# Optimization experiments

Hardware: AMD Instinct MI355X
Metric: run time of the kernel (lower is better)

Reference implementation:

```python
import jax, jax.numpy as jnp
import numpy as np

VOCAB, EMBED, HIDDEN = 32000, 512, 1024
BATCH, SEQ = 32, 48
PAD = 0


def setup_inputs() -> dict:
    key = jax.random.key(0)
    ks = jax.random.split(key, 10)
    s = 0.02
    emb = jax.random.normal(ks[0], (VOCAB, EMBED), jnp.float32) * s
    emb = emb.at[PAD].set(0.0)  # padding_idx row zeroed
    return {
        "inputs": jax.random.randint(ks[1], (BATCH, SEQ), 0, VOCAB),
        "hidden": jax.random.normal(ks[2], (BATCH, HIDDEN), jnp.float32),
        "cell": jax.random.normal(ks[3], (BATCH, HIDDEN), jnp.float32),
        "emb": emb,
        "W_ih": jax.random.normal(ks[4], (4 * HIDDEN, EMBED), jnp.float32) * s,
        "W_hh": jax.random.normal(ks[5], (4 * HIDDEN, HIDDEN), jnp.float32) * s,
        "b_ih": jnp.zeros((4 * HIDDEN,), jnp.float32),
        "b_hh": jnp.zeros((4 * HIDDEN,), jnp.float32),
        "fc_W": jax.random.normal(ks[6], (VOCAB, HIDDEN), jnp.float32) * s,
        "fc_b": jnp.zeros((VOCAB,), jnp.float32),
        "generate_len": 50,
    }


def reference(inputs, hidden, cell, emb, W_ih, W_hh, b_ih, b_hh, fc_W, fc_b, generate_len):
    # Training-path forward (dropout treated as identity for determinism).
    x = emb[inputs]                      # [B, S, E]
    xs = jnp.transpose(x, (1, 0, 2))     # [S, B, E] time-major

    def step(carry, x_t):
        h, c = carry
        gates = x_t @ W_ih.T + b_ih + h @ W_hh.T + b_hh  # [B, 4H]
        i, f, g, o = jnp.split(gates, 4, axis=-1)
        c_new = jax.nn.sigmoid(f) * c + jax.nn.sigmoid(i) * jnp.tanh(g)
        h_new = jax.nn.sigmoid(o) * jnp.tanh(c_new)
        logits = h_new @ fc_W.T + fc_b                   # [B, V]
        return (h_new, c_new), logits

    _, out = jax.lax.scan(step, (hidden, cell), xs)      # [S, B, V]
    return jnp.transpose(out, (1, 0, 2))                 # [B, S, V]
```

## Files before the change

### kernel.cpp

```cpp
#include <hip/hip_runtime.h>
#include <stdint.h>


typedef unsigned short u16;
typedef __attribute__((ext_vector_type(8))) short bf16x8;
typedef __attribute__((ext_vector_type(4))) float floatx4;
struct alignas(8) us4 { u16 x, y, z, w; };

#define BATCH 32
#define SEQ   48
#define EMBED 512
#define HID   1024
#define VOCAB 32000
#define MROWS (SEQ * BATCH)

__device__ __forceinline__ u16 f2bf(float f) {
  unsigned u = __float_as_uint(f);
  u += 0x7FFF + ((u >> 16) & 1);
  return (u16)(u >> 16);
}

__device__ __forceinline__ floatx4 mfma16(bf16x8 a, bf16x8 b, floatx4 c) {
  return __builtin_amdgcn_mfma_f32_16x16x32_bf16(a, b, c, 0, 0, 0);
}

typedef __attribute__((address_space(1))) unsigned int as1_uint;
typedef __attribute__((address_space(3))) unsigned int as3_uint;
__device__ __forceinline__ void gl_lds16(const void* g, void* l) {
  __builtin_amdgcn_global_load_lds((as1_uint*)g, (as3_uint*)l, 16, 0, 0);
}

__device__ __forceinline__ float sigmoidf_(float x) {
  return 1.0f / (1.0f + __expf(-x));
}

__device__ __forceinline__ void ld_c16(bf16x8& d, const u16* p) {
  asm volatile("global_load_dwordx4 %0, %1, off sc0 sc1" : "=&v"(d) : "v"(p));
}
__device__ __forceinline__ void ld_n16(bf16x8& d, const u16* p) {
  asm volatile("global_load_dwordx4 %0, %1, off" : "=&v"(d) : "v"(p));
}

#define BAR_U32S 576

__global__ void cast_all_kernel(const float* __restrict__ s0, u16* __restrict__ d0, int n0,
                                const float* __restrict__ s1, u16* __restrict__ d1, int n1,
                                const float* __restrict__ s2, u16* __restrict__ d2, int n2,
                                const float* __restrict__ s3, u16* __restrict__ d3, int n3) {
  int i = blockIdx.x * blockDim.x + threadIdx.x;
  const float* src; u16* dst; int off;
  if (i < n0)                     { src = s0; dst = d0; off = i; }
  else if (i < n0 + n1)           { src = s1; dst = d1; off = i - n0; }
  else if (i < n0 + n1 + n2)      { src = s2; dst = d2; off = i - n0 - n1; }
  else if (i < n0 + n1 + n2 + n3) { src = s3; dst = d3; off = i - n0 - n1 - n2; }
  else return;
  float4 v = *(const float4*)(src + (size_t)off * 4);
  us4 o;
  o.x = f2bf(v.x); o.y = f2bf(v.y); o.z = f2bf(v.z); o.w = f2bf(v.w);
  *(us4*)(dst + (size_t)off * 4) = o;
}

__global__ void gather_kernel(const int* __restrict__ idx, const float* __restrict__ emb,
                              u16* __restrict__ X, unsigned* __restrict__ bar) {
  int bid = blockIdx.x;
  if (bid == 0) {
    for (int j = threadIdx.x; j < BAR_U32S; j += 128) bar[j] = 0u;
  }
  int s = bid >> 5, b = bid & 31;
  int t = idx[b * SEQ + s];
  const float* src = emb + (size_t)t * EMBED;
  u16* dst = X + (size_t)bid * EMBED;
  int e = threadIdx.x * 4;
  float4 v = *(const float4*)(src + e);
  us4 o;
  o.x = f2bf(v.x); o.y = f2bf(v.y); o.z = f2bf(v.z); o.w = f2bf(v.w);
  *(us4*)(dst + e) = o;
}

__global__ __launch_bounds__(256) void gemm_bt_kernel(
    const u16* __restrict__ A, const u16* __restrict__ B,
    const float* __restrict__ bias0, const float* __restrict__ bias1,
    float* __restrict__ C, int M, int N, int K) {
  __shared__ u16 As[128 * 64];
  __shared__ u16 Bs[128 * 64];

  const int tid = threadIdx.x;
  const int wave = tid >> 6, lane = tid & 63;
  const int l3 = lane >> 3, l7 = lane & 7;
  const int q = lane >> 4, rf = lane & 15;
  const int tn = blockIdx.x, tm = blockIdx.y;
  const int gm0 = tm * 128, gn0 = tn * 128;
  const int wm = (wave & 1) * 64, wn = (wave >> 1) * 64;

  floatx4 acc[4][4];
#pragma unroll
  for (int i = 0; i < 4; ++i)
#pragma unroll
    for (int j = 0; j < 4; ++j) acc[i][j] = (floatx4){0.f, 0.f, 0.f, 0.f};

  for (int k0 = 0; k0 < K; k0 += 64) {
#pragma unroll
    for (int i = 0; i < 4; ++i) {
      int e = wave * 4 + i;
      int r = e * 8 + l3;
      int qd = l7 ^ (r & 7);
      gl_lds16(A + (size_t)(gm0 + r) * K + k0 + qd * 8, (void*)(As + e * 512));
      gl_lds16(B + (size_t)(gn0 + r) * K + k0 + qd * 8, (void*)(Bs + e * 512));
    }
    __syncthreads();

#pragma unroll
    for (int kk = 0; kk < 64; kk += 32) {
      int jc = (kk >> 3) + q;
      bf16x8 af[4], bf[4];
#pragma unroll
      for (int mi = 0; mi < 4; ++mi) {
        int r = wm + mi * 16 + rf;
        af[mi] = *(const bf16x8*)(As + r * 64 + (jc ^ (r & 7)) * 8);
      }
#pragma unroll
      for (int ni = 0; ni < 4; ++ni) {
        int r = wn + ni * 16 + rf;
        bf[ni] = *(const bf16x8*)(Bs + r * 64 + (jc ^ (r & 7)) * 8);
      }
#pragma unroll
      for (int mi = 0; mi < 4; ++mi)
#pragma unroll
        for (int ni = 0; ni < 4; ++ni)
          acc[mi][ni] = mfma16(af[mi], bf[ni], acc[mi][ni]);
    }
    __syncthreads();
  }

#pragma unroll
  for (int ni = 0; ni < 4; ++ni) {
    int n = gn0 + wn + ni * 16 + rf;
    float bv = bias0[n];
    if (bias1) bv += bias1[n];
#pragma unroll
    for (int mi = 0; mi < 4; ++mi) {
#pragma unroll
      for (int r = 0; r < 4; ++r) {
        int m = gm0 + wm + mi * 16 + q * 4 + r;
        C[(size_t)m * N + n] = acc[mi][ni][r] + bv;
      }
    }
  }
}

__global__ __launch_bounds__(512) void gemm_bt256_kernel(
    const u16* __restrict__ A, const u16* __restrict__ B,
    const float* __restrict__ bias0, float* __restrict__ C,
    int N, int K) {
  __shared__ u16 As[256 * 64];
  __shared__ u16 Bs[128 * 64];

  const int tid = threadIdx.x;
  const int wave = tid >> 6, lane = tid & 63;
  const int l3 = lane >> 3, l7 = lane & 7;
  const int q = lane >> 4, rf = lane & 15;
  const int tn = blockIdx.x, tm = blockIdx.y;
  const int gm0 = tm * 256, gn0 = tn * 128;
  const int wm = (wave & 3) * 64, wn = (wave >> 2) * 64;

  floatx4 acc[4][4];
#pragma unroll
  for (int i = 0; i < 4; ++i)
#pragma unroll
    for (int j = 0; j < 4; ++j) acc[i][j] = (floatx4){0.f, 0.f, 0.f, 0.f};

  for (int k0 = 0; k0 < K; k0 += 64) {
#pragma unroll
    for (int i = 0; i < 6; ++i) {
      int e = wave * 6 + i;
      if (e < 32) {
        int r = e * 8 + l3;
        int qd = l7 ^ (r & 7);
        gl_lds16(A + (size_t)(gm0 + r) * K + k0 + qd * 8, (void*)(As + e * 512));
      } else {
        int e2 = e - 32;
        int r = e2 * 8 + l3;
        int qd = l7 ^ (r & 7);
        gl_lds16(B + (size_t)(gn0 + r) * K + k0 + qd * 8, (void*)(Bs + e2 * 512));
      }
    }
    __syncthreads();

#pragma unroll
    for (int kk = 0; kk < 64; kk += 32) {
      int jc = (kk >> 3) + q;
      bf16x8 af[4], bf[4];
#pragma unroll
      for (int mi = 0; mi < 4; ++mi) {
        int r = wm + mi * 16 + rf;
        af[mi] = *(const bf16x8*)(As + r * 64 + (jc ^ (r & 7)) * 8);
      }
#pragma unroll
      for (int ni = 0; ni < 4; ++ni) {
        int r = wn + ni * 16 + rf;
        bf[ni] = *(const bf16x8*)(Bs + r * 64 + (jc ^ (r & 7)) * 8);
      }
#pragma unroll
      for (int mi = 0; mi < 4; ++mi)
#pragma unroll
        for (int ni = 0; ni < 4; ++ni)
          acc[mi][ni] = mfma16(af[mi], bf[ni], acc[mi][ni]);
    }
    __syncthreads();
  }

#pragma unroll
  for (int ni = 0; ni < 4; ++ni) {
    int n = gn0 + wn + ni * 16 + rf;
    float bv = bias0[n];
#pragma unroll
    for (int mi = 0; mi < 4; ++mi) {
#pragma unroll
      for (int r = 0; r < 4; ++r) {
        int m = gm0 + wm + mi * 16 + q * 4 + r;
        int b = m & 31, s = m >> 5;
        C[((size_t)b * SEQ + s) * N + n] = acc[mi][ni][r] + bv;
      }
    }
  }
}

__global__ __launch_bounds__(256, 1) void lstm_persist4_kernel(
    const u16* __restrict__ Whh,
    const float* __restrict__ xg_all,
    const float* __restrict__ c_init,
    u16* __restrict__ Hall,
    unsigned* __restrict__ bar) {
  const int bid = blockIdx.x;
  const int u0 = bid * 4;
  const int tid = threadIdx.x;
  const int wave = tid >> 6, lane = tid & 63;
  const int q = lane >> 4, rf = lane & 15;
  const int gate = rf >> 2, du = rf & 3;
  const int brow = gate * HID + u0 + du;

  __shared__ float red[4][32][16];

  const int ab = tid >> 2, ad = tid & 3;
  float c_reg = 0.f;
  if (tid < 128) c_reg = c_init[ab * HID + u0 + ad];

  const u16* wp = Whh + (size_t)brow * HID + wave * 256 + q * 8;
  bf16x8 wv[8];
#pragma unroll
  for (int i = 0; i < 8; ++i) ld_n16(wv[i], wp + i * 32);

  float xgv[4];
  if (tid < 128) {
#pragma unroll
    for (int gt = 0; gt < 4; ++gt) xgv[gt] = xg_all[ab * 4096 + gt * HID + u0 + ad];
  }

  unsigned* gcnt    = bar + (bid & 7) * 64;
  unsigned* root    = bar + 512;
  unsigned* release = bar + 544;

  for (int s = 0; s < SEQ; ++s) {
    if (s > 0) {
      if (tid == 0) {
        while (__hip_atomic_load(release, __ATOMIC_RELAXED,
                                 __HIP_MEMORY_SCOPE_AGENT) < (unsigned)s)
          __builtin_amdgcn_s_sleep(2);
      }
      __syncthreads();
    }

    const u16* a0p = Hall + (size_t)s * BATCH * HID + (size_t)rf * HID + wave * 256 + q * 8;
    const u16* a1p = a0p + 16 * HID;
    bf16x8 a0v[8], a1v[8];
#pragma unroll
    for (int i = 0; i < 8; ++i) {
      ld_c16(a0v[i], a0p + i * 32);
      ld_c16(a1v[i], a1p + i * 32);
    }
    asm volatile("s_waitcnt vmcnt(0)" ::: "memory");
    __builtin_amdgcn_sched_barrier(0);

    floatx4 acc0 = {0.f, 0.f, 0.f, 0.f}, acc1 = {0.f, 0.f, 0.f, 0.f};
#pragma unroll
    for (int i = 0; i < 8; ++i) {
      acc0 = mfma16(a0v[i], wv[i], acc0);
      acc1 = mfma16(a1v[i], wv[i], acc1);
    }

#pragma unroll
    for (int r = 0; r < 4; ++r) {
      red[wave][q * 4 + r][rf] = acc0[r];
      red[wave][16 + q * 4 + r][rf] = acc1[r];
    }
    __syncthreads();

    if (tid < 128) {
      float g4[4];
#pragma unroll
      for (int gt = 0; gt < 4; ++gt) {
        int n = gt * 4 + ad;
        float v = red[0][ab][n] + red[1][ab][n] + red[2][ab][n] + red[3][ab][n];
        g4[gt] = v + xgv[gt];
      }
      float i_ = sigmoidf_(g4[0]);
      float f_ = sigmoidf_(g4[1]);
      float gg = tanhf(g4[2]);
      float o_ = sigmoidf_(g4[3]);
      c_reg = f_ * c_reg + i_ * gg;
      float hv = o_ * tanhf(c_reg);
      u16 hb = f2bf(hv);
      float hn = __shfl_xor(hv, 1);
      u16 nb = f2bf(hn);
      if ((tid & 1) == 0) {
        unsigned w = (unsigned)hb | ((unsigned)nb << 16);
        unsigned* dst = (unsigned*)(Hall + (size_t)(s + 1) * BATCH * HID +
                                    ab * HID + u0 + ad);
        __hip_atomic_store(dst, w, __ATOMIC_RELAXED, __HIP_MEMORY_SCOPE_AGENT);
      }
    }
    __syncthreads();

    if (s < SEQ - 1) {
      if (tid == 0) {
        unsigned old = __hip_atomic_fetch_add(gcnt, 1u, __ATOMIC_RELAXED,
                                              __HIP_MEMORY_SCOPE_AGENT);
        if (old + 1 == 32u * (unsigned)(s + 1)) {
          unsigned r = __hip_atomic_fetch_add(root, 1u, __ATOMIC_RELAXED,
                                              __HIP_MEMORY_SCOPE_AGENT);
          if (r + 1 == 8u * (unsigned)(s + 1)) {
            __hip_atomic_store(release, (unsigned)(s + 1), __ATOMIC_RELAXED,
                               __HIP_MEMORY_SCOPE_AGENT);
          }
        }
      }
      if (tid < 128) {
        const float* xgn = xg_all + (size_t)(s + 1) * BATCH * 4096;
#pragma unroll
        for (int gt = 0; gt < 4; ++gt) xgv[gt] = xgn[ab * 4096 + gt * HID + u0 + ad];
      }
    }
  }
}

extern "C" void kernel_launch(void* const* d_in, const int* in_sizes, int n_in,
                              void* d_out, int out_size, void* d_ws, size_t ws_size,
                              hipStream_t stream) {
  const int*   inputs = (const int*)d_in[0];
  const float* hidden = (const float*)d_in[1];
  const float* cell   = (const float*)d_in[2];
  const float* emb    = (const float*)d_in[3];
  const float* W_ih   = (const float*)d_in[4];
  const float* W_hh   = (const float*)d_in[5];
  const float* b_ih   = (const float*)d_in[6];
  const float* b_hh   = (const float*)d_in[7];
  const float* fc_W   = (const float*)d_in[8];
  const float* fc_b   = (const float*)d_in[9];
  float* out = (float*)d_out;

  char* ws = (char*)d_ws;
  u16*   Xbf  = (u16*)(ws);
  u16*   Wihb = (u16*)(ws + 1572864);
  u16*   Whhb = (u16*)(ws + 1572864 + 4194304);
  u16*   fcWb = (u16*)(ws + 14155776);
  float* Xg   = (float*)(ws + 14155776 + 65536000);
  u16*   Hall = (u16*)(ws + 104857600);
  unsigned* bar = (unsigned*)(ws + 104857600 + 3211264);

  const int n0 = 4096 * 512 / 4, n1 = 4096 * 1024 / 4,
            n2 = VOCAB * 1024 / 4, n3 = BATCH * HID / 4;
  const int ncast = n0 + n1 + n2 + n3;
  cast_all_kernel<<<(ncast + 255) / 256, 256, 0, stream>>>(
      W_ih, Wihb, n0, W_hh, Whhb, n1, fc_W, fcWb, n2, hidden, Hall, n3);

  gather_kernel<<<MROWS, 128, 0, stream>>>(inputs, emb, Xbf, bar);

  gemm_bt_kernel<<<dim3(4096 / 128, MROWS / 128), 256, 0, stream>>>(
      Xbf, Wihb, b_ih, b_hh, Xg, MROWS, 4096, EMBED);

  lstm_persist4_kernel<<<256, 256, 0, stream>>>(Whhb, Xg, cell, Hall, bar);

  gemm_bt256_kernel<<<dim3(VOCAB / 128, MROWS / 256), 512, 0, stream>>>(
      Hall + (size_t)BATCH * HID, fcWb, fc_b, out, VOCAB, HID);
}
```

Before: 723.8 us.

## Overlap fc_W bf16 cast with persistent LSTM recurrence and tighten barrier

Moves the fc_W fp32-to-bf16 conversion (32000x1024) out of the standalone cast kernel and spreads it across the 48 steps of the persistent LSTM kernel. Each block loads a slice of fc_W before the barrier and stores it after, so the memory traffic hides in the latency-bound recurrence. The change also spins without s_sleep on the release flag, uses an acquire fence with normal loads instead of cache-bypassing sc0/sc1 loads, and switches to rcp-based sigmoid/tanh approximations. The extra loads and stores may contend with the critical-path h loads, and the fast math slightly changes numerics.

```diff
diff --git a/kernel.cpp b/kernel.cpp
--- a/kernel.cpp
+++ b/kernel.cpp
@@ -14,6 +14,9 @@
 #define VOCAB 32000
 #define MROWS (SEQ * BATCH)
 
+#define FCW_F4    8192000
+#define CAST_STEP 196608
+
 __device__ __forceinline__ u16 f2bf(float f) {
   unsigned u = __float_as_uint(f);
   u += 0x7FFF + ((u >> 16) & 1);
@@ -30,29 +33,28 @@
   __builtin_amdgcn_global_load_lds((as1_uint*)g, (as3_uint*)l, 16, 0, 0);
 }
 
-__device__ __forceinline__ float sigmoidf_(float x) {
-  return 1.0f / (1.0f + __expf(-x));
-}
-
-__device__ __forceinline__ void ld_c16(bf16x8& d, const u16* p) {
-  asm volatile("global_load_dwordx4 %0, %1, off sc0 sc1" : "=&v"(d) : "v"(p));
-}
+__device__ __forceinline__ float rcp_(float x) { return __builtin_amdgcn_rcpf(x); }
+__device__ __forceinline__ float sig_(float x) { return rcp_(1.0f + __expf(-x)); }
+__device__ __forceinline__ float tanh_(float x) {
+  float xc = fminf(15.f, fmaxf(-15.f, x));
+  float e = __expf(-2.0f * xc);
+  return (1.0f - e) * rcp_(1.0f + e);
+}
+
 __device__ __forceinline__ void ld_n16(bf16x8& d, const u16* p) {
   asm volatile("global_load_dwordx4 %0, %1, off" : "=&v"(d) : "v"(p));
 }
 
 #define BAR_U32S 576
 
-__global__ void cast_all_kernel(const float* __restrict__ s0, u16* __restrict__ d0, int n0,
-                                const float* __restrict__ s1, u16* __restrict__ d1, int n1,
-                                const float* __restrict__ s2, u16* __restrict__ d2, int n2,
-                                const float* __restrict__ s3, u16* __restrict__ d3, int n3) {
+__global__ void cast3_kernel(const float* __restrict__ s0, u16* __restrict__ d0, int n0,
+                             const float* __restrict__ s1, u16* __restrict__ d1, int n1,
+                             const float* __restrict__ s2, u16* __restrict__ d2, int n2) {
   int i = blockIdx.x * blockDim.x + threadIdx.x;
   const float* src; u16* dst; int off;
-  if (i < n0)                     { src = s0; dst = d0; off = i; }
-  else if (i < n0 + n1)           { src = s1; dst = d1; off = i - n0; }
-  else if (i < n0 + n1 + n2)      { src = s2; dst = d2; off = i - n0 - n1; }
-  else if (i < n0 + n1 + n2 + n3) { src = s3; dst = d3; off = i - n0 - n1 - n2; }
+  if (i < n0)                { src = s0; dst = d0; off = i; }
+  else if (i < n0 + n1)      { src = s1; dst = d1; off = i - n0; }
+  else if (i < n0 + n1 + n2) { src = s2; dst = d2; off = i - n0 - n1; }
   else return;
   float4 v = *(const float4*)(src + (size_t)off * 4);
   us4 o;
@@ -225,12 +227,28 @@
   }
 }
 
-__global__ __launch_bounds__(256, 1) void lstm_persist4_kernel(
+__device__ __forceinline__ void cast_store(const float4* cv, int pend,
+                                           u16* __restrict__ dst) {
+#pragma unroll
+  for (int k = 0; k < 3; ++k) {
+    int i = pend + k * 65536;
+    if (i < FCW_F4) {
+      us4 o;
+      o.x = f2bf(cv[k].x); o.y = f2bf(cv[k].y);
+      o.z = f2bf(cv[k].z); o.w = f2bf(cv[k].w);
+      *(us4*)(dst + (size_t)i * 4) = o;
+    }
+  }
+}
+
+__global__ __launch_bounds__(256, 1) void lstm_persist5_kernel(
     const u16* __restrict__ Whh,
     const float* __restrict__ xg_all,
     const float* __restrict__ c_init,
     u16* __restrict__ Hall,
-    unsigned* __restrict__ bar) {
+    unsigned* __restrict__ bar,
+    const float* __restrict__ fcw_src,
+    u16* __restrict__ fcw_dst) {
   const int bid = blockIdx.x;
   const int u0 = bid * 4;
   const int tid = threadIdx.x;
@@ -256,6 +274,14 @@
     for (int gt = 0; gt < 4; ++gt) xgv[gt] = xg_all[ab * 4096 + gt * HID + u0 + ad];
   }
 
+  float4 cv[3];
+  int pend = 47 * CAST_STEP + bid * 256 + tid;
+#pragma unroll
+  for (int k = 0; k < 3; ++k) {
+    int i = pend + k * 65536;
+    if (i < FCW_F4) cv[k] = *(const float4*)(fcw_src + (size_t)i * 4);
+  }
+
   unsigned* gcnt    = bar + (bid & 7) * 64;
   unsigned* root    = bar + 512;
   unsigned* release = bar + 544;
@@ -264,10 +290,10 @@
     if (s > 0) {
       if (tid == 0) {
         while (__hip_atomic_load(release, __ATOMIC_RELAXED,
-                                 __HIP_MEMORY_SCOPE_AGENT) < (unsigned)s)
-          __builtin_amdgcn_s_sleep(2);
+                                 __HIP_MEMORY_SCOPE_AGENT) < (unsigned)s) { }
       }
       __syncthreads();
+      __builtin_amdgcn_fence(__ATOMIC_ACQUIRE, "agent");
     }
 
     const u16* a0p = Hall + (size_t)s * BATCH * HID + (size_t)rf * HID + wave * 256 + q * 8;
@@ -275,8 +301,8 @@
     bf16x8 a0v[8], a1v[8];
 #pragma unroll
     for (int i = 0; i < 8; ++i) {
-      ld_c16(a0v[i], a0p + i * 32);
-      ld_c16(a1v[i], a1p + i * 32);
+      ld_n16(a0v[i], a0p + i * 32);
+      ld_n16(a1v[i], a1p + i * 32);
     }
     asm volatile("s_waitcnt vmcnt(0)" ::: "memory");
     __builtin_amdgcn_sched_barrier(0);
@@ -303,12 +329,12 @@
         float v = red[0][ab][n] + red[1][ab][n] + red[2][ab][n] + red[3][ab][n];
         g4[gt] = v + xgv[gt];
       }
-      float i_ = sigmoidf_(g4[0]);
-      float f_ = sigmoidf_(g4[1]);
-      float gg = tanhf(g4[2]);
-      float o_ = sigmoidf_(g4[3]);
+      float i_ = sig_(g4[0]);
+      float f_ = sig_(g4[1]);
+      float gg = tanh_(g4[2]);
+      float o_ = sig_(g4[3]);
       c_reg = f_ * c_reg + i_ * gg;
-      float hv = o_ * tanhf(c_reg);
+      float hv = o_ * tanh_(c_reg);
       u16 hb = f2bf(hv);
       float hn = __shfl_xor(hv, 1);
       u16 nb = f2bf(hn);
@@ -334,6 +360,13 @@
           }
         }
       }
+      cast_store(cv, pend, fcw_dst);
+      pend = s * CAST_STEP + bid * 256 + tid;
+#pragma unroll
+      for (int k = 0; k < 3; ++k) {
+        int i = pend + k * 65536;
+        if (i < FCW_F4) cv[k] = *(const float4*)(fcw_src + (size_t)i * 4);
+      }
       if (tid < 128) {
         const float* xgn = xg_all + (size_t)(s + 1) * BATCH * 4096;
 #pragma unroll
@@ -341,6 +374,7 @@
       }
     }
   }
+  cast_store(cv, pend, fcw_dst);
 }
 
 extern "C" void kernel_launch(void* const* d_in, const int* in_sizes, int n_in,
@@ -367,18 +401,18 @@
   u16*   Hall = (u16*)(ws + 104857600);
   unsigned* bar = (unsigned*)(ws + 104857600 + 3211264);
 
-  const int n0 = 4096 * 512 / 4, n1 = 4096 * 1024 / 4,
-            n2 = VOCAB * 1024 / 4, n3 = BATCH * HID / 4;
-  const int ncast = n0 + n1 + n2 + n3;
-  cast_all_kernel<<<(ncast + 255) / 256, 256, 0, stream>>>(
-      W_ih, Wihb, n0, W_hh, Whhb, n1, fc_W, fcWb, n2, hidden, Hall, n3);
+  const int n0 = 4096 * 512 / 4, n1 = 4096 * 1024 / 4, n2 = BATCH * HID / 4;
+  const int ncast = n0 + n1 + n2;
+  cast3_kernel<<<(ncast + 255) / 256, 256, 0, stream>>>(
+      W_ih, Wihb, n0, W_hh, Whhb, n1, hidden, Hall, n2);
 
   gather_kernel<<<MROWS, 128, 0, stream>>>(inputs, emb, Xbf, bar);
 
   gemm_bt_kernel<<<dim3(4096 / 128, MROWS / 128), 256, 0, stream>>>(
       Xbf, Wihb, b_ih, b_hh, Xg, MROWS, 4096, EMBED);
 
-  lstm_persist4_kernel<<<256, 256, 0, stream>>>(Whhb, Xg, cell, Hall, bar);
+  lstm_persist5_kernel<<<256, 256, 0, stream>>>(Whhb, Xg, cell, Hall, bar,
+                                                fc_W, fcWb);
 
   gemm_bt256_kernel<<<dim3(VOCAB / 128, MROWS / 256), 512, 0, stream>>>(
       Hall + (size_t)BATCH * HID, fcWb, fc_b, out, VOCAB, HID);
```

Result: slower. 1.005 ms (+38.8%).
